# Kernel tuning notes

Measured on AMD Instinct MI355X. Metric: run time of the kernel, lower is better.

The kernel has to match this reference:

```python
import jax, jax.numpy as jnp
import numpy as np

N, C, H, DIN = 200_000, 16, 64, 40  # nodes in level, max children, hidden_dim, input_dim+type_count
NEG = -1e9

def setup_inputs() -> dict:
    key = jax.random.key(0)
    ks = jax.random.split(key, 10)
    s = lambda k, shp, f=0.1: jax.random.normal(k, shp, jnp.float32) * f
    return {
        'node_features': jax.random.normal(ks[0], (N, 1, DIN), jnp.float32),
        'child_hiddens': jax.random.normal(ks[1], (N, C, H), jnp.float32),
        'A_c': jax.random.uniform(ks[2], (N, C, C), jnp.float32),  # edge present where > 0.5
        'child_count': jax.random.randint(ks[3], (N,), 1, C + 1, jnp.int32),
        'W': s(ks[4], (H, H)),
        'a_src': s(ks[5], (H,)),
        'a_dst': s(ks[6], (H,)),
        'Wx': s(ks[7], (DIN, 3 * H)),
        'Wh_g': s(ks[8], (H, 3 * H)),
        'b': jnp.zeros((3 * H,), jnp.float32),
    }

def reference(node_features, child_hiddens, A_c, child_count, W, a_src, a_dst, Wx, Wh_g, b):
    # --- GraphAttentionLayer over padded child adjacency ---
    Wh = jnp.einsum('nch,hk->nck', child_hiddens, W)            # [N,C,H]
    src = Wh @ a_src                                             # [N,C]
    dst = Wh @ a_dst                                             # [N,C]
    e = jax.nn.leaky_relu(src[:, :, None] + dst[:, None, :], 0.2)  # [N,C,C]
    valid = jnp.arange(C)[None, :] < child_count[:, None]        # [N,C] real (non-padded) children
    mask = (A_c > 0.5) & valid[:, None, :] & valid[:, :, None]
    attn = jax.nn.softmax(jnp.where(mask, e, NEG), axis=-1)
    h_msg = jax.nn.elu(jnp.einsum('nij,njh->nih', attn, Wh))     # [N,C,H]
    # --- MaxpoolReadoutLayer masked by child count ---
    pooled = jnp.max(jnp.where(valid[:, :, None], h_msg, NEG), axis=1, keepdims=True)  # [N,1,H]
    # --- GatedRecurrentUnit update ---
    gx = node_features @ Wx + b                                  # [N,1,3H]
    gh = pooled @ Wh_g                                           # [N,1,3H]
    xz, xr, xn = jnp.split(gx, 3, axis=-1)
    hz, hr, hn = jnp.split(gh, 3, axis=-1)
    z = jax.nn.sigmoid(xz + hz)
    r = jax.nn.sigmoid(xr + hr)
    n = jnp.tanh(xn + r * hn)
    hiddens = (1.0 - z) * n + z * pooled                         # [N,1,H]
    return hiddens
```

## Files before the change

kernel.cpp:

```cpp
#include <hip/hip_runtime.h>

typedef __attribute__((ext_vector_type(8))) short bf16x8;
typedef __attribute__((ext_vector_type(4))) float f32x4;

__device__ __forceinline__ unsigned short f2bf(float f) {
  unsigned u = __builtin_bit_cast(unsigned, f);
  u += 0x7fffu + ((u >> 16) & 1u);
  return (unsigned short)(u >> 16);
}
__device__ __forceinline__ float bf2f(unsigned short s) {
  unsigned u = ((unsigned)s) << 16;
  return __builtin_bit_cast(float, u);
}
__device__ __forceinline__ bf16x8 zero8() {
  bf16x8 r;
#pragma unroll
  for (int i = 0; i < 8; ++i) r[i] = 0;
  return r;
}

__global__ __launch_bounds__(256, 2) void rann_fused(
    const float* __restrict__ nf, const float* __restrict__ ch,
    const float* __restrict__ Ac, const int* __restrict__ ccnt,
    const float* __restrict__ W, const float* __restrict__ a_src,
    const float* __restrict__ a_dst, const float* __restrict__ Wx,
    const float* __restrict__ Whg, const float* __restrict__ bias,
    float* __restrict__ out, int N) {
  __shared__ __align__(16) unsigned short whgT[192][72];
  __shared__ __align__(16) unsigned short wxT[192][72];
  __shared__ __align__(16) float b_lds[192];
  __shared__ __align__(16) float srcdst[4][32];
  __shared__ __align__(16) unsigned short wh_t[4][64][16];
  __shared__ __align__(16) unsigned short pooledb[4][16][72];

  const int tid = threadIdx.x;
  for (int idx = tid; idx < 192 * 64; idx += 256) {
    const int col = idx % 192, k = idx / 192;
    whgT[col][k] = f2bf(Whg[k * 192 + col]);
    wxT[col][k] = (k < 40) ? f2bf(Wx[k * 192 + col]) : (unsigned short)0;
  }
  if (tid < 192) b_lds[tid] = bias[tid];
  __syncthreads();

  const int lane = tid & 63;
  const int w = tid >> 6;
  const int q = lane >> 4;
  const int m16 = lane & 15;

  bf16x8 wfrag[2][4];
#pragma unroll
  for (int t = 0; t < 2; ++t)
#pragma unroll
    for (int u = 0; u < 4; ++u) {
      bf16x8 f;
#pragma unroll
      for (int j = 0; j < 8; ++j)
        f[j] = (short)f2bf(W[(32 * t + 8 * q + j) * 64 + 16 * u + m16]);
      wfrag[t][u] = f;
    }
  float asv[4], adv[4];
#pragma unroll
  for (int u = 0; u < 4; ++u) {
    asv[u] = a_src[16 * u + m16];
    adv[u] = a_dst[16 * u + m16];
  }

  const int gwave = blockIdx.x * 4 + w;
  const int stride = gridDim.x * 4;
  const int nbatch = N >> 4;
  for (int bidx = gwave; bidx < nbatch; bidx += stride) {
    const int nb = bidx << 4;
    for (int s = 0; s < 16; ++s) {
      const int n = nb + s;
      const int cc = ccnt[n];
      bf16x8 afA[2];
#pragma unroll
      for (int t = 0; t < 2; ++t) {
        const float* p = ch + (size_t)n * 1024 + m16 * 64 + 32 * t + 8 * q;
        f32x4 v0 = *(const f32x4*)p;
        f32x4 v1 = *(const f32x4*)(p + 4);
        bf16x8 f;
#pragma unroll
        for (int j = 0; j < 4; ++j) {
          f[j] = (short)f2bf(v0[j]);
          f[j + 4] = (short)f2bf(v1[j]);
        }
        afA[t] = f;
      }
      f32x4 acc[4];
#pragma unroll
      for (int u = 0; u < 4; ++u) acc[u] = (f32x4){0.f, 0.f, 0.f, 0.f};
#pragma unroll
      for (int t = 0; t < 2; ++t)
#pragma unroll
        for (int u = 0; u < 4; ++u)
          acc[u] = __builtin_amdgcn_mfma_f32_16x16x32_bf16(afA[t], wfrag[t][u], acc[u], 0, 0, 0);

      float ps[4], pd[4];
#pragma unroll
      for (int r = 0; r < 4; ++r) {
        ps[r] = acc[0][r] * asv[0] + acc[1][r] * asv[1] + acc[2][r] * asv[2] + acc[3][r] * asv[3];
        pd[r] = acc[0][r] * adv[0] + acc[1][r] * adv[1] + acc[2][r] * adv[2] + acc[3][r] * adv[3];
      }
#pragma unroll
      for (int m = 1; m < 16; m <<= 1) {
#pragma unroll
        for (int r = 0; r < 4; ++r) {
          ps[r] += __shfl_xor(ps[r], m);
          pd[r] += __shfl_xor(pd[r], m);
        }
      }
      if (m16 == 0) {
        *(f32x4*)&srcdst[w][4 * q] = (f32x4){ps[0], ps[1], ps[2], ps[3]};
        *(f32x4*)&srcdst[w][16 + 4 * q] = (f32x4){pd[0], pd[1], pd[2], pd[3]};
      }
#pragma unroll
      for (int u = 0; u < 4; ++u) {
        uint2 v;
        v.x = (unsigned)f2bf(acc[u][0]) | ((unsigned)f2bf(acc[u][1]) << 16);
        v.y = (unsigned)f2bf(acc[u][2]) | ((unsigned)f2bf(acc[u][3]) << 16);
        *(uint2*)&wh_t[w][16 * u + m16][4 * q] = v;
      }
      __threadfence_block();

      const int qe = q & 1;
      const float srcv = srcdst[w][m16];
      f32x4 d0 = *(const f32x4*)&srcdst[w][16 + 8 * qe];
      f32x4 d1 = *(const f32x4*)&srcdst[w][16 + 8 * qe + 4];
      const float* ap = Ac + (size_t)n * 256 + m16 * 16 + 8 * qe;
      f32x4 a0 = *(const f32x4*)ap;
      f32x4 a1 = *(const f32x4*)(ap + 4);
      float p8[8];
      float rmax = -3.0e38f;
#pragma unroll
      for (int jj = 0; jj < 8; ++jj) {
        const float dstv = (jj < 4) ? d0[jj] : d1[jj - 4];
        const float av = (jj < 4) ? a0[jj] : a1[jj - 4];
        const float x = srcv + dstv;
        const float e = fmaxf(x, 0.2f * x);
        const bool msk = (av > 0.5f) && (m16 < cc) && ((8 * qe + jj) < cc);
        p8[jj] = msk ? e : -1.0e9f;
        rmax = fmaxf(rmax, p8[jj]);
      }
      rmax = fmaxf(rmax, __shfl_xor(rmax, 16));
      float psum = 0.f;
#pragma unroll
      for (int jj = 0; jj < 8; ++jj) {
        p8[jj] = __expf(p8[jj] - rmax);
        psum += p8[jj];
      }
      psum += __shfl_xor(psum, 16);
      const float inv = 1.0f / psum;
      bf16x8 afrag2 = zero8();
      if (q < 2) {
#pragma unroll
        for (int jj = 0; jj < 8; ++jj) afrag2[jj] = (short)f2bf(p8[jj] * inv);
      }
      f32x4 acc2[4];
#pragma unroll
      for (int u = 0; u < 4; ++u) {
        bf16x8 bf2 = zero8();
        if (q < 2) bf2 = *(const bf16x8*)&wh_t[w][16 * u + m16][8 * q];
        f32x4 z4 = (f32x4){0.f, 0.f, 0.f, 0.f};
        acc2[u] = __builtin_amdgcn_mfma_f32_16x16x32_bf16(afrag2, bf2, z4, 0, 0, 0);
      }
#pragma unroll
      for (int u = 0; u < 4; ++u) {
        float pm = -1.0e9f;
#pragma unroll
        for (int r = 0; r < 4; ++r) {
          const float v = acc2[u][r];
          const float ev = v > 0.f ? v : __expf(v) - 1.0f;
          pm = fmaxf(pm, (4 * q + r) < cc ? ev : -1.0e9f);
        }
        pm = fmaxf(pm, __shfl_xor(pm, 16));
        pm = fmaxf(pm, __shfl_xor(pm, 32));
        if (q == 0) pooledb[w][s][16 * u + m16] = f2bf(pm);
      }
    }
    __threadfence_block();

    bf16x8 afP[2];
#pragma unroll
    for (int t = 0; t < 2; ++t)
      afP[t] = *(const bf16x8*)&pooledb[w][m16][32 * t + 8 * q];
    bf16x8 afX[2];
    {
      const float* p = nf + (size_t)(nb + m16) * 40 + 8 * q;
      f32x4 v0 = *(const f32x4*)p;
      f32x4 v1 = *(const f32x4*)(p + 4);
      bf16x8 f;
#pragma unroll
      for (int j = 0; j < 4; ++j) {
        f[j] = (short)f2bf(v0[j]);
        f[j + 4] = (short)f2bf(v1[j]);
      }
      afX[0] = f;
      afX[1] = zero8();
      if (q == 0) {
        const float* p1 = nf + (size_t)(nb + m16) * 40 + 32;
        f32x4 w0 = *(const f32x4*)p1;
        f32x4 w1 = *(const f32x4*)(p1 + 4);
        bf16x8 g;
#pragma unroll
        for (int j = 0; j < 4; ++j) {
          g[j] = (short)f2bf(w0[j]);
          g[j + 4] = (short)f2bf(w1[j]);
        }
        afX[1] = g;
      }
    }
    f32x4 accS[8], accX4[4], accH4[4];
#pragma unroll
    for (int u = 0; u < 8; ++u) accS[u] = (f32x4){0.f, 0.f, 0.f, 0.f};
#pragma unroll
    for (int u = 0; u < 4; ++u) {
      accX4[u] = (f32x4){0.f, 0.f, 0.f, 0.f};
      accH4[u] = (f32x4){0.f, 0.f, 0.f, 0.f};
    }
#pragma unroll
    for (int u = 0; u < 8; ++u) {
      const int row = 16 * u + m16;
#pragma unroll
      for (int t = 0; t < 2; ++t) {
        accS[u] = __builtin_amdgcn_mfma_f32_16x16x32_bf16(
            afP[t], *(const bf16x8*)&whgT[row][32 * t + 8 * q], accS[u], 0, 0, 0);
        accS[u] = __builtin_amdgcn_mfma_f32_16x16x32_bf16(
            afX[t], *(const bf16x8*)&wxT[row][32 * t + 8 * q], accS[u], 0, 0, 0);
      }
    }
#pragma unroll
    for (int u = 0; u < 4; ++u) {
      const int row = 128 + 16 * u + m16;
#pragma unroll
      for (int t = 0; t < 2; ++t) {
        accH4[u] = __builtin_amdgcn_mfma_f32_16x16x32_bf16(
            afP[t], *(const bf16x8*)&whgT[row][32 * t + 8 * q], accH4[u], 0, 0, 0);
        accX4[u] = __builtin_amdgcn_mfma_f32_16x16x32_bf16(
            afX[t], *(const bf16x8*)&wxT[row][32 * t + 8 * q], accX4[u], 0, 0, 0);
      }
    }
#pragma unroll
    for (int u = 0; u < 4; ++u) {
      const int col = 16 * u + m16;
      const float bz = b_lds[col];
      const float br = b_lds[64 + col];
      const float bn = b_lds[128 + col];
#pragma unroll
      for (int r = 0; r < 4; ++r) {
        const int nl = 4 * q + r;
        const float z = 1.0f / (1.0f + __expf(-(accS[u][r] + bz)));
        const float rg = 1.0f / (1.0f + __expf(-(accS[u + 4][r] + br)));
        const float nn = tanhf(accX4[u][r] + bn + rg * accH4[u][r]);
        const float pv = bf2f(pooledb[w][nl][col]);
        out[(size_t)(nb + nl) * 64 + col] = (1.0f - z) * nn + z * pv;
      }
    }
  }
}

extern "C" void kernel_launch(void* const* d_in, const int* in_sizes, int n_in,
                              void* d_out, int out_size, void* d_ws, size_t ws_size,
                              hipStream_t stream) {
  const float* nf = (const float*)d_in[0];
  const float* ch = (const float*)d_in[1];
  const float* Ac = (const float*)d_in[2];
  const int* ccnt = (const int*)d_in[3];
  const float* W = (const float*)d_in[4];
  const float* a_src = (const float*)d_in[5];
  const float* a_dst = (const float*)d_in[6];
  const float* Wx = (const float*)d_in[7];
  const float* Whg = (const float*)d_in[8];
  const float* bias = (const float*)d_in[9];
  float* out = (float*)d_out;
  const int N = in_sizes[3];
  const int nbatch = N >> 4;
  int blocks = 625;
  if (blocks > (nbatch + 3) / 4) blocks = (nbatch + 3) / 4;
  if (blocks < 1) blocks = 1;
  hipLaunchKernelGGL(rann_fused, dim3(blocks), dim3(256), 0, stream,
                     nf, ch, Ac, ccnt, W, a_src, a_dst, Wx, Whg, bias, out, N);
}
```

Baseline: 1.496 ms.

## Prefetch child tiles, fold attention vectors into MFMA, drop LDS weights, dynamic scheduling

Several changes land together. The next node's child_hiddens tile is now prefetched while the current one is processed, and src/dst scores come from an extra MFMA against W·a_src and W·a_dst instead of shuffle reductions. The GRU weight staging in LDS is removed so weights are read from global/L2, which shrinks LDS use, and occupancy is raised to 4 blocks with 1024 blocks pulling batches from an atomic work counter. tanh is replaced with a clamped exp formula, and the fences become lgkmcnt waits. The costs are repeated global weight loads per batch, higher register pressure from the prefetch, and precomputing W·a in bf16, which changes rounding.

```diff
diff --git a/kernel.cpp b/kernel.cpp
--- a/kernel.cpp
+++ b/kernel.cpp
@@ -18,34 +18,40 @@
   for (int i = 0; i < 8; ++i) r[i] = 0;
   return r;
 }
-
-__global__ __launch_bounds__(256, 2) void rann_fused(
+__device__ __forceinline__ bf16x8 cvt8(f32x4 a, f32x4 b) {
+  bf16x8 f;
+#pragma unroll
+  for (int j = 0; j < 4; ++j) {
+    f[j] = (short)f2bf(a[j]);
+    f[j + 4] = (short)f2bf(b[j]);
+  }
+  return f;
+}
+__device__ __forceinline__ bf16x8 ldBf(const float* __restrict__ M, int k0, int col) {
+  bf16x8 f;
+#pragma unroll
+  for (int j = 0; j < 8; ++j) f[j] = (short)f2bf(M[(k0 + j) * 192 + col]);
+  return f;
+}
+#define LGKM0() asm volatile("s_waitcnt lgkmcnt(0)" ::: "memory")
+
+__global__ __launch_bounds__(256, 4) void rann_fused(
     const float* __restrict__ nf, const float* __restrict__ ch,
     const float* __restrict__ Ac, const int* __restrict__ ccnt,
     const float* __restrict__ W, const float* __restrict__ a_src,
     const float* __restrict__ a_dst, const float* __restrict__ Wx,
     const float* __restrict__ Whg, const float* __restrict__ bias,
-    float* __restrict__ out, int N) {
-  __shared__ __align__(16) unsigned short whgT[192][72];
-  __shared__ __align__(16) unsigned short wxT[192][72];
-  __shared__ __align__(16) float b_lds[192];
+    float* __restrict__ out, int N, int* counter, int nbatch) {
   __shared__ __align__(16) float srcdst[4][32];
   __shared__ __align__(16) unsigned short wh_t[4][64][16];
-  __shared__ __align__(16) unsigned short pooledb[4][16][72];
+  __shared__ __align__(16) unsigned short pooledb[4][16][64];
 
   const int tid = threadIdx.x;
-  for (int idx = tid; idx < 192 * 64; idx += 256) {
-    const int col = idx % 192, k = idx / 192;
-    whgT[col][k] = f2bf(Whg[k * 192 + col]);
-    wxT[col][k] = (k < 40) ? f2bf(Wx[k * 192 + col]) : (unsigned short)0;
-  }
-  if (tid < 192) b_lds[tid] = bias[tid];
-  __syncthreads();
-
   const int lane = tid & 63;
   const int w = tid >> 6;
   const int q = lane >> 4;
   const int m16 = lane & 15;
+  const int qe = q & 1;
 
   bf16x8 wfrag[2][4];
 #pragma unroll
@@ -58,62 +64,76 @@
         f[j] = (short)f2bf(W[(32 * t + 8 * q + j) * 64 + 16 * u + m16]);
       wfrag[t][u] = f;
     }
-  float asv[4], adv[4];
-#pragma unroll
-  for (int u = 0; u < 4; ++u) {
-    asv[u] = a_src[16 * u + m16];
-    adv[u] = a_dst[16 * u + m16];
-  }
-
-  const int gwave = blockIdx.x * 4 + w;
-  const int stride = gridDim.x * 4;
-  const int nbatch = N >> 4;
-  for (int bidx = gwave; bidx < nbatch; bidx += stride) {
+  float was = 0.f, wad = 0.f;
+  for (int h = 0; h < 64; ++h) {
+    const float wv = W[lane * 64 + h];
+    was += wv * a_src[h];
+    wad += wv * a_dst[h];
+  }
+  bf16x8 bsd[2];
+#pragma unroll
+  for (int t = 0; t < 2; ++t) {
+    bf16x8 f;
+#pragma unroll
+    for (int j = 0; j < 8; ++j) {
+      const int k = 32 * t + 8 * q + j;
+      const float vs = __shfl(was, k);
+      const float vd = __shfl(wad, k);
+      f[j] = (m16 == 0) ? (short)f2bf(vs) : ((m16 == 1) ? (short)f2bf(vd) : (short)0);
+    }
+    bsd[t] = f;
+  }
+
+  int next_static = blockIdx.x * 4 + w;
+  for (;;) {
+    int bidx;
+    if (counter) {
+      if (lane == 0) bidx = atomicAdd(counter, 1);
+      bidx = __shfl(bidx, 0);
+    } else {
+      bidx = next_static;
+      next_static += gridDim.x * 4;
+    }
+    if (bidx >= nbatch) break;
     const int nb = bidx << 4;
+
+    f32x4 chv[4];
+    {
+      const float* p = ch + (size_t)nb * 1024 + m16 * 64 + 8 * q;
+      chv[0] = *(const f32x4*)p;
+      chv[1] = *(const f32x4*)(p + 4);
+      chv[2] = *(const f32x4*)(p + 32);
+      chv[3] = *(const f32x4*)(p + 36);
+    }
     for (int s = 0; s < 16; ++s) {
-      const int n = nb + s;
-      const int cc = ccnt[n];
-      bf16x8 afA[2];
-#pragma unroll
-      for (int t = 0; t < 2; ++t) {
-        const float* p = ch + (size_t)n * 1024 + m16 * 64 + 32 * t + 8 * q;
-        f32x4 v0 = *(const f32x4*)p;
-        f32x4 v1 = *(const f32x4*)(p + 4);
-        bf16x8 f;
-#pragma unroll
-        for (int j = 0; j < 4; ++j) {
-          f[j] = (short)f2bf(v0[j]);
-          f[j + 4] = (short)f2bf(v1[j]);
-        }
-        afA[t] = f;
-      }
+      f32x4 chn[4];
+      if (s < 15) {
+        const float* p = ch + (size_t)(nb + s + 1) * 1024 + m16 * 64 + 8 * q;
+        chn[0] = *(const f32x4*)p;
+        chn[1] = *(const f32x4*)(p + 4);
+        chn[2] = *(const f32x4*)(p + 32);
+        chn[3] = *(const f32x4*)(p + 36);
+      }
+      const float* ap = Ac + (size_t)(nb + s) * 256 + m16 * 16 + 8 * qe;
+      const f32x4 ac0 = *(const f32x4*)ap;
+      const f32x4 ac1 = *(const f32x4*)(ap + 4);
+      const int cc = ccnt[nb + s];
+
+      const bf16x8 afA0 = cvt8(chv[0], chv[1]);
+      const bf16x8 afA1 = cvt8(chv[2], chv[3]);
       f32x4 acc[4];
 #pragma unroll
       for (int u = 0; u < 4; ++u) acc[u] = (f32x4){0.f, 0.f, 0.f, 0.f};
 #pragma unroll
-      for (int t = 0; t < 2; ++t)
-#pragma unroll
-        for (int u = 0; u < 4; ++u)
-          acc[u] = __builtin_amdgcn_mfma_f32_16x16x32_bf16(afA[t], wfrag[t][u], acc[u], 0, 0, 0);
-
-      float ps[4], pd[4];
-#pragma unroll
-      for (int r = 0; r < 4; ++r) {
-        ps[r] = acc[0][r] * asv[0] + acc[1][r] * asv[1] + acc[2][r] * asv[2] + acc[3][r] * asv[3];
-        pd[r] = acc[0][r] * adv[0] + acc[1][r] * adv[1] + acc[2][r] * adv[2] + acc[3][r] * adv[3];
-      }
-#pragma unroll
-      for (int m = 1; m < 16; m <<= 1) {
-#pragma unroll
-        for (int r = 0; r < 4; ++r) {
-          ps[r] += __shfl_xor(ps[r], m);
-          pd[r] += __shfl_xor(pd[r], m);
-        }
-      }
-      if (m16 == 0) {
-        *(f32x4*)&srcdst[w][4 * q] = (f32x4){ps[0], ps[1], ps[2], ps[3]};
-        *(f32x4*)&srcdst[w][16 + 4 * q] = (f32x4){pd[0], pd[1], pd[2], pd[3]};
-      }
+      for (int u = 0; u < 4; ++u) {
+        acc[u] = __builtin_amdgcn_mfma_f32_16x16x32_bf16(afA0, wfrag[0][u], acc[u], 0, 0, 0);
+        acc[u] = __builtin_amdgcn_mfma_f32_16x16x32_bf16(afA1, wfrag[1][u], acc[u], 0, 0, 0);
+      }
+      f32x4 sd = (f32x4){0.f, 0.f, 0.f, 0.f};
+      sd = __builtin_amdgcn_mfma_f32_16x16x32_bf16(afA0, bsd[0], sd, 0, 0, 0);
+      sd = __builtin_amdgcn_mfma_f32_16x16x32_bf16(afA1, bsd[1], sd, 0, 0, 0);
+      if (m16 < 2) *(f32x4*)&srcdst[w][16 * m16 + 4 * q] = sd;
+
 #pragma unroll
       for (int u = 0; u < 4; ++u) {
         uint2 v;
@@ -121,21 +141,17 @@
         v.y = (unsigned)f2bf(acc[u][2]) | ((unsigned)f2bf(acc[u][3]) << 16);
         *(uint2*)&wh_t[w][16 * u + m16][4 * q] = v;
       }
-      __threadfence_block();
-
-      const int qe = q & 1;
+      LGKM0();
+
       const float srcv = srcdst[w][m16];
-      f32x4 d0 = *(const f32x4*)&srcdst[w][16 + 8 * qe];
-      f32x4 d1 = *(const f32x4*)&srcdst[w][16 + 8 * qe + 4];
-      const float* ap = Ac + (size_t)n * 256 + m16 * 16 + 8 * qe;
-      f32x4 a0 = *(const f32x4*)ap;
-      f32x4 a1 = *(const f32x4*)(ap + 4);
+      const f32x4 d0 = *(const f32x4*)&srcdst[w][16 + 8 * qe];
+      const f32x4 d1 = *(const f32x4*)&srcdst[w][16 + 8 * qe + 4];
       float p8[8];
       float rmax = -3.0e38f;
 #pragma unroll
       for (int jj = 0; jj < 8; ++jj) {
         const float dstv = (jj < 4) ? d0[jj] : d1[jj - 4];
-        const float av = (jj < 4) ? a0[jj] : a1[jj - 4];
+        const float av = (jj < 4) ? ac0[jj] : ac1[jj - 4];
         const float x = srcv + dstv;
         const float e = fmaxf(x, 0.2f * x);
         const bool msk = (av > 0.5f) && (m16 < cc) && ((8 * qe + jj) < cc);
@@ -161,7 +177,7 @@
       for (int u = 0; u < 4; ++u) {
         bf16x8 bf2 = zero8();
         if (q < 2) bf2 = *(const bf16x8*)&wh_t[w][16 * u + m16][8 * q];
-        f32x4 z4 = (f32x4){0.f, 0.f, 0.f, 0.f};
+        const f32x4 z4 = (f32x4){0.f, 0.f, 0.f, 0.f};
         acc2[u] = __builtin_amdgcn_mfma_f32_16x16x32_bf16(afrag2, bf2, z4, 0, 0, 0);
       }
 #pragma unroll
@@ -177,81 +193,67 @@
         pm = fmaxf(pm, __shfl_xor(pm, 32));
         if (q == 0) pooledb[w][s][16 * u + m16] = f2bf(pm);
       }
-    }
-    __threadfence_block();
+      if (s < 15) {
+        chv[0] = chn[0]; chv[1] = chn[1]; chv[2] = chn[2]; chv[3] = chn[3];
+      }
+    }
+    LGKM0();
 
     bf16x8 afP[2];
 #pragma unroll
     for (int t = 0; t < 2; ++t)
       afP[t] = *(const bf16x8*)&pooledb[w][m16][32 * t + 8 * q];
-    bf16x8 afX[2];
+    bf16x8 afX0, afX1;
     {
       const float* p = nf + (size_t)(nb + m16) * 40 + 8 * q;
-      f32x4 v0 = *(const f32x4*)p;
-      f32x4 v1 = *(const f32x4*)(p + 4);
-      bf16x8 f;
-#pragma unroll
-      for (int j = 0; j < 4; ++j) {
-        f[j] = (short)f2bf(v0[j]);
-        f[j + 4] = (short)f2bf(v1[j]);
-      }
-      afX[0] = f;
-      afX[1] = zero8();
+      afX0 = cvt8(*(const f32x4*)p, *(const f32x4*)(p + 4));
+      afX1 = zero8();
       if (q == 0) {
         const float* p1 = nf + (size_t)(nb + m16) * 40 + 32;
-        f32x4 w0 = *(const f32x4*)p1;
-        f32x4 w1 = *(const f32x4*)(p1 + 4);
-        bf16x8 g;
-#pragma unroll
-        for (int j = 0; j < 4; ++j) {
-          g[j] = (short)f2bf(w0[j]);
-          g[j + 4] = (short)f2bf(w1[j]);
-        }
-        afX[1] = g;
-      }
-    }
-    f32x4 accS[8], accX4[4], accH4[4];
+        afX1 = cvt8(*(const f32x4*)p1, *(const f32x4*)(p1 + 4));
+      }
+    }
+    f32x4 accS[8], accNh[4], accNx[4];
 #pragma unroll
     for (int u = 0; u < 8; ++u) accS[u] = (f32x4){0.f, 0.f, 0.f, 0.f};
 #pragma unroll
     for (int u = 0; u < 4; ++u) {
-      accX4[u] = (f32x4){0.f, 0.f, 0.f, 0.f};
-      accH4[u] = (f32x4){0.f, 0.f, 0.f, 0.f};
+      accNh[u] = (f32x4){0.f, 0.f, 0.f, 0.f};
+      accNx[u] = (f32x4){0.f, 0.f, 0.f, 0.f};
     }
 #pragma unroll
     for (int u = 0; u < 8; ++u) {
-      const int row = 16 * u + m16;
-#pragma unroll
-      for (int t = 0; t < 2; ++t) {
-        accS[u] = __builtin_amdgcn_mfma_f32_16x16x32_bf16(
-            afP[t], *(const bf16x8*)&whgT[row][32 * t + 8 * q], accS[u], 0, 0, 0);
-        accS[u] = __builtin_amdgcn_mfma_f32_16x16x32_bf16(
-            afX[t], *(const bf16x8*)&wxT[row][32 * t + 8 * q], accS[u], 0, 0, 0);
-      }
-    }
-#pragma unroll
-    for (int u = 0; u < 4; ++u) {
-      const int row = 128 + 16 * u + m16;
-#pragma unroll
-      for (int t = 0; t < 2; ++t) {
-        accH4[u] = __builtin_amdgcn_mfma_f32_16x16x32_bf16(
-            afP[t], *(const bf16x8*)&whgT[row][32 * t + 8 * q], accH4[u], 0, 0, 0);
-        accX4[u] = __builtin_amdgcn_mfma_f32_16x16x32_bf16(
-            afX[t], *(const bf16x8*)&wxT[row][32 * t + 8 * q], accX4[u], 0, 0, 0);
-      }
-    }
-#pragma unroll
-    for (int u = 0; u < 4; ++u) {
       const int col = 16 * u + m16;
-      const float bz = b_lds[col];
-      const float br = b_lds[64 + col];
-      const float bn = b_lds[128 + col];
+      accS[u] = __builtin_amdgcn_mfma_f32_16x16x32_bf16(afP[0], ldBf(Whg, 8 * q, col), accS[u], 0, 0, 0);
+      accS[u] = __builtin_amdgcn_mfma_f32_16x16x32_bf16(afP[1], ldBf(Whg, 32 + 8 * q, col), accS[u], 0, 0, 0);
+      accS[u] = __builtin_amdgcn_mfma_f32_16x16x32_bf16(afX0, ldBf(Wx, 8 * q, col), accS[u], 0, 0, 0);
+      const bf16x8 bx1 = (q == 0) ? ldBf(Wx, 32, col) : zero8();
+      accS[u] = __builtin_amdgcn_mfma_f32_16x16x32_bf16(afX1, bx1, accS[u], 0, 0, 0);
+    }
+#pragma unroll
+    for (int u = 0; u < 4; ++u) {
+      const int col = 128 + 16 * u + m16;
+      accNh[u] = __builtin_amdgcn_mfma_f32_16x16x32_bf16(afP[0], ldBf(Whg, 8 * q, col), accNh[u], 0, 0, 0);
+      accNh[u] = __builtin_amdgcn_mfma_f32_16x16x32_bf16(afP[1], ldBf(Whg, 32 + 8 * q, col), accNh[u], 0, 0, 0);
+      accNx[u] = __builtin_amdgcn_mfma_f32_16x16x32_bf16(afX0, ldBf(Wx, 8 * q, col), accNx[u], 0, 0, 0);
+      const bf16x8 bx1 = (q == 0) ? ldBf(Wx, 32, col) : zero8();
+      accNx[u] = __builtin_amdgcn_mfma_f32_16x16x32_bf16(afX1, bx1, accNx[u], 0, 0, 0);
+    }
+#pragma unroll
+    for (int u = 0; u < 4; ++u) {
+      const int col = 16 * u + m16;
+      const float bz = bias[col];
+      const float br = bias[64 + col];
+      const float bn = bias[128 + col];
 #pragma unroll
       for (int r = 0; r < 4; ++r) {
         const int nl = 4 * q + r;
         const float z = 1.0f / (1.0f + __expf(-(accS[u][r] + bz)));
         const float rg = 1.0f / (1.0f + __expf(-(accS[u + 4][r] + br)));
-        const float nn = tanhf(accX4[u][r] + bn + rg * accH4[u][r]);
+        float xv = accNx[u][r] + bn + rg * accNh[u][r];
+        xv = fminf(fmaxf(xv, -15.f), 15.f);
+        const float t2 = __expf(2.f * xv);
+        const float nn = (t2 - 1.f) / (t2 + 1.f);
         const float pv = bf2f(pooledb[w][nl][col]);
         out[(size_t)(nb + nl) * 64 + col] = (1.0f - z) * nn + z * pv;
       }
@@ -275,9 +277,12 @@
   float* out = (float*)d_out;
   const int N = in_sizes[3];
   const int nbatch = N >> 4;
-  int blocks = 625;
-  if (blocks > (nbatch + 3) / 4) blocks = (nbatch + 3) / 4;
-  if (blocks < 1) blocks = 1;
-  hipLaunchKernelGGL(rann_fused, dim3(blocks), dim3(256), 0, stream,
-                     nf, ch, Ac, ccnt, W, a_src, a_dst, Wx, Whg, bias, out, N);
-}
+  int* counter = nullptr;
+  if (ws_size >= sizeof(int)) {
+    counter = (int*)d_ws;
+    hipMemsetAsync(d_ws, 0, sizeof(int), stream);
+  }
+  hipLaunchKernelGGL(rann_fused, dim3(1024), dim3(256), 0, stream,
+                     nf, ch, Ac, ccnt, W, a_src, a_dst, Wx, Whg, bias, out, N,
+                     counter, nbatch);
+}
```

New measurement: 1.935 ms. 29.4% more time.
